# Kernel tuning notes

Measured on AMD Instinct MI355X. Metric: run time of the kernel, lower is better.

Reference implementation:

```python
import jax, jax.numpy as jnp
import numpy as np
import math

EPS = 1e-12  # F.normalize default eps

def _l2_normalize(x):
    n = jnp.sqrt(jnp.sum(x * x, axis=-1, keepdims=True))
    return x / jnp.maximum(n, EPS)

def setup_inputs() -> dict:
    key = jax.random.key(0)
    k1, k2 = jax.random.split(key)
    B, F, C = 16384, 1024, 1000
    features = jax.random.normal(k1, (B, F), dtype=jnp.float32)
    prototypes = jax.random.normal(k2, (C, F), dtype=jnp.float32)
    distance_scale = jnp.ones((1,), dtype=jnp.float32)
    temperature = jnp.ones((1,), dtype=jnp.float32)
    return {"features": features, "prototypes": prototypes,
            "distance_scale": distance_scale, "temperature": temperature}

def reference(features, prototypes, distance_scale, temperature):
    # L2-normalize both sides (F.normalize, p=2, eps=1e-12)
    f = _l2_normalize(features)      # [B, F]
    p = _l2_normalize(prototypes)    # [C, F]
    # Pairwise Euclidean distance. For unit vectors ||f-p||^2 = 2 - 2 f.p,
    # clamped at 0 for numerical safety; then / sqrt(2).
    sim = jnp.einsum('bf,cf->bc', f, p)                  # [B, C]
    sq = jnp.maximum(2.0 - 2.0 * sim, 0.0)
    distances = jnp.sqrt(sq) / jnp.float32(math.sqrt(2.0))
    iso = jnp.abs(distance_scale) * distances            # [B, C]
    logits = -(iso + jnp.mean(iso, axis=1, keepdims=True))
    return logits / temperature
```

## Files before the change

kernel.cpp:

```cpp
#include <hip/hip_runtime.h>
#include <hip/hip_bf16.h>
#include <math.h>

#define B_ROWS 16384
#define C_COLS 1000
#define C_PAD  1024
#define FDIM   1024
#define FBLKS  4096

typedef __attribute__((ext_vector_type(8))) short bf16x8;
typedef __attribute__((ext_vector_type(4))) float f32x4;

#define GLD_LDS(gp, lp) __builtin_amdgcn_global_load_lds( \
    (__attribute__((address_space(1))) void*)(gp),        \
    (__attribute__((address_space(3))) void*)(lp), 16, 0, 0)

__global__ __launch_bounds__(256) void normalize_all(
    const float* __restrict__ feat, const float* __restrict__ prot,
    __hip_bfloat16* __restrict__ fb, __hip_bfloat16* __restrict__ pb)
{
    const int lane = threadIdx.x & 63;
    const int wave = threadIdx.x >> 6;

    const float* in;
    __hip_bfloat16* out;
    int row, nvalid;
    if (blockIdx.x < FBLKS) {
        row = blockIdx.x * 4 + wave;  in = feat; out = fb; nvalid = B_ROWS;
    } else {
        row = (blockIdx.x - FBLKS) * 4 + wave;  in = prot; out = pb; nvalid = C_COLS;
    }
    __hip_bfloat16* orow = out + (size_t)row * FDIM;

    if (row >= nvalid) {
        ushort4 z = make_ushort4(0, 0, 0, 0);
        #pragma unroll
        for (int c = 0; c < 4; ++c) ((ushort4*)orow)[lane + c * 64] = z;
        return;
    }

    const float4* rp = (const float4*)(in + (size_t)row * FDIM);
    float4 v[4];
    float ss = 0.0f;
    #pragma unroll
    for (int c = 0; c < 4; ++c) {
        v[c] = rp[lane + c * 64];
        ss += v[c].x * v[c].x + v[c].y * v[c].y + v[c].z * v[c].z + v[c].w * v[c].w;
    }
    #pragma unroll
    for (int off = 1; off < 64; off <<= 1) ss += __shfl_xor(ss, off, 64);
    const float inv = 1.0f / sqrtf(fmaxf(ss, 1e-24f));

    #pragma unroll
    for (int c = 0; c < 4; ++c) {
        __hip_bfloat16 o[4];
        o[0] = __float2bfloat16(v[c].x * inv);
        o[1] = __float2bfloat16(v[c].y * inv);
        o[2] = __float2bfloat16(v[c].z * inv);
        o[3] = __float2bfloat16(v[c].w * inv);
        ((ushort4*)orow)[lane + c * 64] = *(ushort4*)o;
    }
}

__global__ __launch_bounds__(256) void gemm_dist(
    const __hip_bfloat16* __restrict__ A,
    const __hip_bfloat16* __restrict__ Bp,
    __hip_bfloat16* __restrict__ D,
    float* __restrict__ rowsum)
{
    __shared__ __hip_bfloat16 As[2][128 * 32];
    __shared__ __hip_bfloat16 Bs[2][128 * 32];

    const int tid  = threadIdx.x;
    const int lane = tid & 63;
    const int wave = tid >> 6;

    const int id  = blockIdx.x;
    const int xcd = id & 7;
    const int seq = id >> 3;
    const int bn  = seq & 7;
    const int bm  = xcd * 16 + (seq >> 3);

    const int waveM = (wave >> 1) * 64;
    const int waveN = (wave & 1) * 64;

    f32x4 acc[4][4] = {};

    const int srow = lane >> 2;
    const int sq   = (lane & 3) ^ ((srow >> 1) & 3);
    const __hip_bfloat16* Abase = A  + ((size_t)(bm * 128) + wave * 32 + srow) * FDIM + sq * 8;
    const __hip_bfloat16* Bbase = Bp + ((size_t)(bn * 128) + wave * 32 + srow) * FDIM + sq * 8;

    #define STAGE(koff, b) do {                                              \
        GLD_LDS(Abase + (size_t)(koff),             &As[b][wave * 1024]);        \
        GLD_LDS(Abase + (size_t)(koff) + 16 * FDIM, &As[b][wave * 1024 + 512]);  \
        GLD_LDS(Bbase + (size_t)(koff),             &Bs[b][wave * 1024]);        \
        GLD_LDS(Bbase + (size_t)(koff) + 16 * FDIM, &Bs[b][wave * 1024 + 512]);  \
    } while (0)

    STAGE(0, 0);
    __syncthreads();

    const int q = lane >> 4;
    #pragma unroll 2
    for (int k = 0; k < 32; ++k) {
        const int cur = k & 1;
        if (k < 31) STAGE((k + 1) * 32, cur ^ 1);

        bf16x8 a[4], b[4];
        #pragma unroll
        for (int mt = 0; mt < 4; ++mt) {
            const int R = waveM + mt * 16 + (lane & 15);
            a[mt] = *(const bf16x8*)&As[cur][R * 32 + ((q ^ ((R >> 1) & 3)) * 8)];
        }
        #pragma unroll
        for (int nt = 0; nt < 4; ++nt) {
            const int R = waveN + nt * 16 + (lane & 15);
            b[nt] = *(const bf16x8*)&Bs[cur][R * 32 + ((q ^ ((R >> 1) & 3)) * 8)];
        }
        #pragma unroll
        for (int mt = 0; mt < 4; ++mt)
            #pragma unroll
            for (int nt = 0; nt < 4; ++nt)
                acc[mt][nt] = __builtin_amdgcn_mfma_f32_16x16x32_bf16(a[mt], b[nt], acc[mt][nt], 0, 0, 0);

        __syncthreads();
    }

    const int row0 = bm * 128 + waveM;
    const int col0 = bn * 128 + waveN;
    #pragma unroll
    for (int mt = 0; mt < 4; ++mt) {
        #pragma unroll
        for (int r = 0; r < 4; ++r) {
            const int row = row0 + mt * 16 + (lane >> 4) * 4 + r;
            float part = 0.0f;
            #pragma unroll
            for (int nt = 0; nt < 4; ++nt) {
                const int col = col0 + nt * 16 + (lane & 15);
                const float sim = acc[mt][nt][r];
                const float dv = sqrtf(fmaxf(1.0f - sim, 0.0f));
                if (col < C_COLS) {
                    D[(size_t)row * C_COLS + col] = __float2bfloat16(dv);
                    part += dv;
                }
            }
            part += __shfl_xor(part, 1, 64);
            part += __shfl_xor(part, 2, 64);
            part += __shfl_xor(part, 4, 64);
            part += __shfl_xor(part, 8, 64);
            if ((lane & 15) == 0) atomicAdd(&rowsum[row], part);
        }
    }
}

__global__ __launch_bounds__(256) void finalize(
    const __hip_bfloat16* __restrict__ D, const float* __restrict__ rowsum,
    const float* __restrict__ scale, const float* __restrict__ temp,
    float* __restrict__ out)
{
    const size_t i = (size_t)blockIdx.x * 256 + threadIdx.x;
    const float a = -fabsf(scale[0]) / temp[0];
    const int row = (int)((i * 8) / C_COLS);
    const float m = rowsum[row] * (1.0f / (float)C_COLS);

    const bf16x8 dv = *(const bf16x8*)(D + i * 8);
    const __hip_bfloat16* dp = (const __hip_bfloat16*)&dv;
    float4 o0, o1;
    o0.x = a * (__bfloat162float(dp[0]) + m);
    o0.y = a * (__bfloat162float(dp[1]) + m);
    o0.z = a * (__bfloat162float(dp[2]) + m);
    o0.w = a * (__bfloat162float(dp[3]) + m);
    o1.x = a * (__bfloat162float(dp[4]) + m);
    o1.y = a * (__bfloat162float(dp[5]) + m);
    o1.z = a * (__bfloat162float(dp[6]) + m);
    o1.w = a * (__bfloat162float(dp[7]) + m);
    ((float4*)out)[i * 2]     = o0;
    ((float4*)out)[i * 2 + 1] = o1;
}

extern "C" void kernel_launch(void* const* d_in, const int* in_sizes, int n_in,
                              void* d_out, int out_size, void* d_ws, size_t ws_size,
                              hipStream_t stream)
{
    const float* features = (const float*)d_in[0];
    const float* protos   = (const float*)d_in[1];
    const float* dscale   = (const float*)d_in[2];
    const float* temp     = (const float*)d_in[3];
    float* out = (float*)d_out;

    char* ws = (char*)d_ws;
    __hip_bfloat16* fb = (__hip_bfloat16*)ws;
    __hip_bfloat16* pb = (__hip_bfloat16*)(ws + 33554432);
    __hip_bfloat16* D  = (__hip_bfloat16*)(ws + 35651584);
    float* rowsum      = (float*)(ws + 68419584);

    hipMemsetAsync(rowsum, 0, B_ROWS * sizeof(float), stream);

    normalize_all<<<FBLKS + C_PAD / 4, 256, 0, stream>>>(features, protos, fb, pb);

    gemm_dist<<<1024, 256, 0, stream>>>(fb, pb, D, rowsum);

    finalize<<<(B_ROWS * C_COLS / 8) / 256, 256, 0, stream>>>(D, rowsum, dscale, temp, out);
}
```

Measured before the change: 192.8 us.

## Quantize normalized operands to scaled FP8 and use MX FP8 MFMA

Normalization now writes FP8 (e4m3) values pre-scaled by 256 instead of bf16, halving the intermediate traffic. The GEMM switches to the 16x16x128 scaled FP8 MFMA with 128-wide K tiles loaded into single-buffered LDS, and rescales the accumulator afterwards. The rowsum memset is folded into the normalize kernel. This risks accuracy loss from FP8 quantization of unit vectors, and the removal of double buffering may expose load latency.

Result: faster. 160.6 us (-16.7%).

```diff
diff --git a/kernel.cpp b/kernel.cpp
--- a/kernel.cpp
+++ b/kernel.cpp
@@ -7,9 +7,13 @@
 #define C_PAD  1024
 #define FDIM   1024
 #define FBLKS  4096
+#define FP8_SCALE 256.0f
+#define INV_SIM   (1.0f / (FP8_SCALE * FP8_SCALE))
 
 typedef __attribute__((ext_vector_type(8))) short bf16x8;
 typedef __attribute__((ext_vector_type(4))) float f32x4;
+typedef __attribute__((ext_vector_type(4))) int   i32x4;
+typedef __attribute__((ext_vector_type(8))) int   i32x8;
 
 #define GLD_LDS(gp, lp) __builtin_amdgcn_global_load_lds( \
     (__attribute__((address_space(1))) void*)(gp),        \
@@ -17,25 +21,27 @@
 
 __global__ __launch_bounds__(256) void normalize_all(
     const float* __restrict__ feat, const float* __restrict__ prot,
-    __hip_bfloat16* __restrict__ fb, __hip_bfloat16* __restrict__ pb)
+    unsigned char* __restrict__ fb, unsigned char* __restrict__ pb,
+    float* __restrict__ rowsum)
 {
     const int lane = threadIdx.x & 63;
     const int wave = threadIdx.x >> 6;
 
+    if (blockIdx.x < 64) rowsum[blockIdx.x * 256 + threadIdx.x] = 0.0f;
+
     const float* in;
-    __hip_bfloat16* out;
+    unsigned char* out;
     int row, nvalid;
     if (blockIdx.x < FBLKS) {
         row = blockIdx.x * 4 + wave;  in = feat; out = fb; nvalid = B_ROWS;
     } else {
         row = (blockIdx.x - FBLKS) * 4 + wave;  in = prot; out = pb; nvalid = C_COLS;
     }
-    __hip_bfloat16* orow = out + (size_t)row * FDIM;
+    unsigned char* orow = out + (size_t)row * FDIM;
 
     if (row >= nvalid) {
-        ushort4 z = make_ushort4(0, 0, 0, 0);
-        #pragma unroll
-        for (int c = 0; c < 4; ++c) ((ushort4*)orow)[lane + c * 64] = z;
+        i32x4 z = {0, 0, 0, 0};
+        ((i32x4*)orow)[lane] = z;
         return;
     }
 
@@ -44,32 +50,31 @@
     float ss = 0.0f;
     #pragma unroll
     for (int c = 0; c < 4; ++c) {
-        v[c] = rp[lane + c * 64];
+        v[c] = rp[lane * 4 + c];
         ss += v[c].x * v[c].x + v[c].y * v[c].y + v[c].z * v[c].z + v[c].w * v[c].w;
     }
     #pragma unroll
     for (int off = 1; off < 64; off <<= 1) ss += __shfl_xor(ss, off, 64);
-    const float inv = 1.0f / sqrtf(fmaxf(ss, 1e-24f));
-
+    const float inv = FP8_SCALE / sqrtf(fmaxf(ss, 1e-24f));
+
+    i32x4 pk;
     #pragma unroll
     for (int c = 0; c < 4; ++c) {
-        __hip_bfloat16 o[4];
-        o[0] = __float2bfloat16(v[c].x * inv);
-        o[1] = __float2bfloat16(v[c].y * inv);
-        o[2] = __float2bfloat16(v[c].z * inv);
-        o[3] = __float2bfloat16(v[c].w * inv);
-        ((ushort4*)orow)[lane + c * 64] = *(ushort4*)o;
-    }
+        int w0 = __builtin_amdgcn_cvt_pk_fp8_f32(v[c].x * inv, v[c].y * inv, 0, false);
+        w0     = __builtin_amdgcn_cvt_pk_fp8_f32(v[c].z * inv, v[c].w * inv, w0, true);
+        pk[c] = w0;
+    }
+    ((i32x4*)orow)[lane] = pk;
 }
 
 __global__ __launch_bounds__(256) void gemm_dist(
-    const __hip_bfloat16* __restrict__ A,
-    const __hip_bfloat16* __restrict__ Bp,
+    const unsigned char* __restrict__ A,
+    const unsigned char* __restrict__ Bp,
     __hip_bfloat16* __restrict__ D,
     float* __restrict__ rowsum)
 {
-    __shared__ __hip_bfloat16 As[2][128 * 32];
-    __shared__ __hip_bfloat16 Bs[2][128 * 32];
+    __shared__ unsigned char As[128 * 128];
+    __shared__ unsigned char Bs[128 * 128];
 
     const int tid  = threadIdx.x;
     const int lane = tid & 63;
@@ -86,45 +91,45 @@
 
     f32x4 acc[4][4] = {};
 
-    const int srow = lane >> 2;
-    const int sq   = (lane & 3) ^ ((srow >> 1) & 3);
-    const __hip_bfloat16* Abase = A  + ((size_t)(bm * 128) + wave * 32 + srow) * FDIM + sq * 8;
-    const __hip_bfloat16* Bbase = Bp + ((size_t)(bn * 128) + wave * 32 + srow) * FDIM + sq * 8;
-
-    #define STAGE(koff, b) do {                                              \
-        GLD_LDS(Abase + (size_t)(koff),             &As[b][wave * 1024]);        \
-        GLD_LDS(Abase + (size_t)(koff) + 16 * FDIM, &As[b][wave * 1024 + 512]);  \
-        GLD_LDS(Bbase + (size_t)(koff),             &Bs[b][wave * 1024]);        \
-        GLD_LDS(Bbase + (size_t)(koff) + 16 * FDIM, &Bs[b][wave * 1024 + 512]);  \
-    } while (0)
-
-    STAGE(0, 0);
-    __syncthreads();
-
-    const int q = lane >> 4;
-    #pragma unroll 2
-    for (int k = 0; k < 32; ++k) {
-        const int cur = k & 1;
-        if (k < 31) STAGE((k + 1) * 32, cur ^ 1);
-
-        bf16x8 a[4], b[4];
+    const int srow8 = lane >> 3;
+    const int sg    = (lane & 7) ^ srow8;
+    const unsigned char* Abase = A  + ((size_t)(bm * 128 + wave * 8 + srow8)) * FDIM + sg * 16;
+    const unsigned char* Bbase = Bp + ((size_t)(bn * 128 + wave * 8 + srow8)) * FDIM + sg * 16;
+
+    const int q2   = (lane >> 4) * 2;
+    const int bxor = lane & 7;
+    const int fA = (waveM + (lane & 15)) * 128;
+    const int fB = (waveN + (lane & 15)) * 128;
+    const int pg0 = ((q2)     ^ bxor) * 16;
+    const int pg1 = ((q2 + 1) ^ bxor) * 16;
+
+    #pragma unroll 1
+    for (int k0 = 0; k0 < FDIM; k0 += 128) {
+        __syncthreads();
+        #pragma unroll
+        for (int r = 0; r < 4; ++r) {
+            GLD_LDS(Abase + (size_t)(r * 32) * FDIM + k0, &As[(r * 32 + wave * 8) * 128]);
+            GLD_LDS(Bbase + (size_t)(r * 32) * FDIM + k0, &Bs[(r * 32 + wave * 8) * 128]);
+        }
+        __syncthreads();
+
+        i32x8 b[4];
+        #pragma unroll
+        for (int nt = 0; nt < 4; ++nt) {
+            const i32x4 lo = *(const i32x4*)&Bs[fB + nt * 2048 + pg0];
+            const i32x4 hi = *(const i32x4*)&Bs[fB + nt * 2048 + pg1];
+            b[nt] = (i32x8){lo.x, lo.y, lo.z, lo.w, hi.x, hi.y, hi.z, hi.w};
+        }
         #pragma unroll
         for (int mt = 0; mt < 4; ++mt) {
-            const int R = waveM + mt * 16 + (lane & 15);
-            a[mt] = *(const bf16x8*)&As[cur][R * 32 + ((q ^ ((R >> 1) & 3)) * 8)];
-        }
-        #pragma unroll
-        for (int nt = 0; nt < 4; ++nt) {
-            const int R = waveN + nt * 16 + (lane & 15);
-            b[nt] = *(const bf16x8*)&Bs[cur][R * 32 + ((q ^ ((R >> 1) & 3)) * 8)];
-        }
-        #pragma unroll
-        for (int mt = 0; mt < 4; ++mt)
+            const i32x4 lo = *(const i32x4*)&As[fA + mt * 2048 + pg0];
+            const i32x4 hi = *(const i32x4*)&As[fA + mt * 2048 + pg1];
+            const i32x8 a = (i32x8){lo.x, lo.y, lo.z, lo.w, hi.x, hi.y, hi.z, hi.w};
             #pragma unroll
             for (int nt = 0; nt < 4; ++nt)
-                acc[mt][nt] = __builtin_amdgcn_mfma_f32_16x16x32_bf16(a[mt], b[nt], acc[mt][nt], 0, 0, 0);
-
-        __syncthreads();
+                acc[mt][nt] = __builtin_amdgcn_mfma_scale_f32_16x16x128_f8f6f4(
+                    a, b[nt], acc[mt][nt], 0, 0, 0, 127, 0, 127);
+        }
     }
 
     const int row0 = bm * 128 + waveM;
@@ -138,7 +143,7 @@
             #pragma unroll
             for (int nt = 0; nt < 4; ++nt) {
                 const int col = col0 + nt * 16 + (lane & 15);
-                const float sim = acc[mt][nt][r];
+                const float sim = acc[mt][nt][r] * INV_SIM;
                 const float dv = sqrtf(fmaxf(1.0f - sim, 0.0f));
                 if (col < C_COLS) {
                     D[(size_t)row * C_COLS + col] = __float2bfloat16(dv);
@@ -190,14 +195,12 @@
     float* out = (float*)d_out;
 
     char* ws = (char*)d_ws;
-    __hip_bfloat16* fb = (__hip_bfloat16*)ws;
-    __hip_bfloat16* pb = (__hip_bfloat16*)(ws + 33554432);
-    __hip_bfloat16* D  = (__hip_bfloat16*)(ws + 35651584);
-    float* rowsum      = (float*)(ws + 68419584);
-
-    hipMemsetAsync(rowsum, 0, B_ROWS * sizeof(float), stream);
-
-    normalize_all<<<FBLKS + C_PAD / 4, 256, 0, stream>>>(features, protos, fb, pb);
+    unsigned char* fb = (unsigned char*)ws;
+    unsigned char* pb = (unsigned char*)(ws + 16777216);
+    __hip_bfloat16* D = (__hip_bfloat16*)(ws + 17825792);
+    float* rowsum     = (float*)(ws + 50593792);
+
+    normalize_all<<<FBLKS + C_PAD / 4, 256, 0, stream>>>(features, protos, fb, pb, rowsum);
 
     gemm_dist<<<1024, 256, 0, stream>>>(fb, pb, D, rowsum);
 
```
